# Kernel tuning notes

Measured on AMD Instinct MI355X. Metric: run time of the kernel, lower is better.

The kernel has to match this reference:

```python
import jax, jax.numpy as jnp
import numpy as np

# ---- static anchor construction (mirrors build_anchors + valid_index in __init__) ----
F_W, F_H, F_S = 50, 37, 16
SCALES = (8.0, 16.0, 24.0)
RATIOS = (0.5, 1.0, 2.0)
K1 = 400            # rp() top-k proposals fed to NMS
NMS_THRESH = 0.6
BN_EPS = 1e-5

def _build_anchors():
    anchors = []
    for y in range(F_H):
        for x in range(F_W):
            cx = x * F_S + F_S / 2.0
            cy = y * F_S + F_S / 2.0
            for r in RATIOS:           # 3 ratios x 3 scales = 9 anchors/cell (18 = 9*2 cls ch)
                for s in SCALES:
                    h = F_S * s * np.sqrt(r)
                    w = F_S * s / np.sqrt(r)
                    anchors.append([cx - w / 2, cy - h / 2, cx + w / 2, cy + h / 2])
    return np.asarray(anchors, dtype=np.float32)

_ANCH = _build_anchors()
_VALID = np.where((_ANCH[:, 0] >= 0) & (_ANCH[:, 1] >= 0) &
                  (_ANCH[:, 2] < F_W * F_S) & (_ANCH[:, 3] < F_H * F_S))[0]
VALID_ANCHOR = jnp.asarray(_ANCH[_VALID])   # [V, 4]
VALID_INDEX = jnp.asarray(_VALID)            # [V]


def _conv(x, w, b, pad):
    y = jax.lax.conv_general_dilated(x, w, (1, 1), [(pad, pad), (pad, pad)],
                                     dimension_numbers=('NCHW', 'OIHW', 'NCHW'))
    return y + b[None, :, None, None]


def _nms_keep(boxes, scores, thresh):
    """Greedy NMS over K1 boxes; returns bool keep mask aligned to input order."""
    n = boxes.shape[0]
    order = jnp.argsort(-scores)
    b = boxes[order]
    x1, y1, x2, y2 = b[:, 0], b[:, 1], b[:, 2], b[:, 3]
    area = (x2 - x1 + 1.0) * (y2 - y1 + 1.0)
    iw = jnp.clip(jnp.minimum(x2[:, None], x2[None, :]) - jnp.maximum(x1[:, None], x1[None, :]) + 1.0, 0.0)
    ih = jnp.clip(jnp.minimum(y2[:, None], y2[None, :]) - jnp.maximum(y1[:, None], y1[None, :]) + 1.0, 0.0)
    inter = iw * ih
    iou = inter / (area[:, None] + area[None, :] - inter)
    idx = jnp.arange(n)

    def body(i, supp):
        alive = ~supp[i]
        new = alive & (iou[i] > thresh) & (idx > i)
        return supp | new

    supp = jax.lax.fori_loop(0, n, body, jnp.zeros(n, dtype=bool))
    return jnp.zeros(n, dtype=bool).at[order].set(~supp)


def _rp_single(off_i, cls_i):
    """rp(): softmax fg score -> top-k1 -> box decode -> NMS keep mask."""
    off_v = off_i[VALID_INDEX]                       # [V, 4]
    cls_v = cls_i[VALID_INDEX]                       # [V, 2]
    score = jax.nn.softmax(cls_v, axis=1)[:, 1]
    top_s, top_idx = jax.lax.top_k(score, K1)
    a = VALID_ANCHOR[top_idx]
    t = off_v[top_idx]
    xa = (a[:, 0] + a[:, 2]) / 2
    ya = (a[:, 1] + a[:, 3]) / 2
    wa = a[:, 2] - a[:, 0] + 1.0
    ha = a[:, 3] - a[:, 1] + 1.0
    x = t[:, 0] * wa + xa
    y = t[:, 1] * ha + ya
    w = wa * jnp.exp(t[:, 2])
    h = ha * jnp.exp(t[:, 3])
    boxes = jnp.stack([x - w / 2, y - h / 2, x + w / 2, y + h / 2], axis=1)  # [K1, 4]
    keep = _nms_keep(jnp.trunc(boxes), top_s, NMS_THRESH)  # original casts to int before NMS
    return boxes, keep


def setup_inputs() -> dict:
    key = jax.random.key(0)
    ks = jax.random.split(key, 8)
    B = 8
    return {
        'feature': jax.random.normal(ks[0], (B, 512, F_H, F_W), jnp.float32),
        'md_w': jax.random.normal(ks[1], (512, 512, 3, 3), jnp.float32) * 0.02,
        'md_b': jax.random.normal(ks[2], (512,), jnp.float32) * 0.01,
        'bn_gamma': jnp.ones((512,), jnp.float32),
        'bn_beta': jnp.zeros((512,), jnp.float32),
        'cls_w': jax.random.normal(ks[3], (18, 512, 1, 1), jnp.float32) * 0.02,
        'cls_b': jax.random.normal(ks[4], (18,), jnp.float32) * 0.01,
        'off_w': jax.random.normal(ks[5], (36, 512, 1, 1), jnp.float32) * 0.02,
        'off_b': jax.random.normal(ks[6], (36,), jnp.float32) * 0.01,
    }


def reference(feature, md_w, md_b, bn_gamma, bn_beta, cls_w, cls_b, off_w, off_b):
    B = feature.shape[0]
    # more_deep: Conv3x3 -> BatchNorm (training-mode batch stats) -> ReLU
    out = _conv(feature, md_w, md_b, pad=1)
    mean = out.mean(axis=(0, 2, 3), keepdims=True)
    var = out.var(axis=(0, 2, 3), keepdims=True)
    out = bn_gamma[None, :, None, None] * (out - mean) * jax.lax.rsqrt(var + BN_EPS) + bn_beta[None, :, None, None]
    out = jax.nn.relu(out)
    # 1x1 heads, then permute(0,2,3,1).reshape as in predict()
    cls = _conv(out, cls_w, cls_b, pad=0)   # [B,18,H,W]
    off = _conv(out, off_w, off_b, pad=0)   # [B,36,H,W]
    cls_pred = cls.transpose(0, 2, 3, 1).reshape(B, -1, 2)   # [B, H*W*9, 2]
    offset_pred = off.transpose(0, 2, 3, 1).reshape(B, -1, 4)  # [B, H*W*9, 4]
    boxes, keep = jax.vmap(_rp_single)(offset_pred, cls_pred)  # [B,K1,4], [B,K1] bool
    return offset_pred, cls_pred, boxes, keep
```

## Files before the change

kernel.cpp:

```cpp
#include <hip/hip_runtime.h>
#include <cstdint>

#define BHW_ 14800
#define CHW_ 947200
#define A_   16650
#define OCLS 532800
#define OBOX 799200
#define OKEEP 812000
#define NSTEP 144

typedef unsigned int u32;
typedef unsigned long long u64;
typedef _Float16 f16x8 __attribute__((ext_vector_type(8)));
typedef float f32x4 __attribute__((ext_vector_type(4)));

__device__ __forceinline__ unsigned int fkey(float f){
  unsigned int u = __float_as_uint(f);
  return (u & 0x80000000u) ? ~u : (u | 0x80000000u);
}

__device__ __forceinline__ void anchor_corners(int x, int y, int kk,
                                               float& ax1, float& ay1, float& ax2, float& ay2){
  int si = kk % 3, ri = kk / 3;
  double rv = (ri==0) ? 0.5 : ((ri==1) ? 1.0 : 2.0);
  double sr = sqrt(rv);
  double fs = 128.0 * (double)(si+1);
  double h = fs * sr, w = fs / sr;
  double cx = (double)(x*16 + 8), cy = (double)(y*16 + 8);
  ax1 = (float)(cx - w*0.5); ay1 = (float)(cy - h*0.5);
  ax2 = (float)(cx + w*0.5); ay2 = (float)(cy + h*0.5);
}

__global__ __launch_bounds__(256) void k_split_w(const float* __restrict__ w,
                                                 const float* __restrict__ cw, const float* __restrict__ cb,
                                                 const float* __restrict__ ow, const float* __restrict__ ob,
                                                 _Float16* __restrict__ WfA,
                                                 float* __restrict__ hwp, float* __restrict__ hb){
  int bid = blockIdx.x;
  if (bid < 1152){
    int u = bid*256 + threadIdx.x;
    int khw = u % 9;
    int v = u / 9;
    int o7  = v & 127;
    int l4g = (v >> 7) & 3;
    int ot  = (v >> 9) & 3;
    int cc  = v >> 11;
    int o = ot*128 + o7;
    int s = cc*9 + khw;
    f16x8 hi, lo;
    #pragma unroll
    for (int j = 0; j < 8; ++j){
      float val = w[(size_t)(o*512 + cc*32 + l4g*8 + j)*9 + khw];
      _Float16 h = (_Float16)val;
      hi[j] = h; lo[j] = (_Float16)(val - (float)h);
    }
    size_t base = ((size_t)(s*4 + ot)*1024 + (size_t)(l4g*2)*128 + o7)*8;
    *(f16x8*)&WfA[base] = hi;
    *(f16x8*)&WfA[base + 1024] = lo;
  } else {
    int t = (bid - 1152)*256 + threadIdx.x;
    if (t < 64) hb[t] = (t < 18) ? cb[t] : (t < 54 ? ob[t-18] : 0.f);
    int r = t & 63, ci = t >> 6;
    hwp[t] = (r < 18) ? cw[r*512 + ci] : (r < 54 ? ow[(r-18)*512 + ci] : 0.f);
  }
}

__global__ __launch_bounds__(256) void k_split_f(const float* __restrict__ feat,
                                                 _Float16* __restrict__ Fph, _Float16* __restrict__ Fpl){
  int bid = blockIdx.x;
  if (bid < 928){
    __shared__ float T[64][129];
    int ct = bid & 3; int pt = (bid >> 2) % 29; int b = bid / 116;
    int tid = threadIdx.x;
    #pragma unroll
    for (int it = 0; it < 32; ++it){
      int idx = it*256 + tid;
      int c = idx >> 6, p = idx & 63;
      int pos = pt*64 + p;
      T[p][c] = (pos < 1850) ? feat[(size_t)(b*512 + ct*128 + c)*1850 + pos] : 0.f;
    }
    __syncthreads();
    #pragma unroll
    for (int it = 0; it < 4; ++it){
      int idx = it*256 + tid;
      int p = idx >> 4, c8 = (idx & 15) * 8;
      int pos = pt*64 + p;
      if (pos < 1850){
        int y = pos/50, x = pos - y*50;
        size_t off = ((size_t)(b*39 + y + 1)*52 + (x + 1))*512 + ct*128 + c8;
        f16x8 hv, lv;
        #pragma unroll
        for (int j = 0; j < 8; ++j){
          float v = T[p][c8 + j];
          _Float16 h = (_Float16)v;
          hv[j] = h; lv[j] = (_Float16)(v - (float)h);
        }
        *(f16x8*)&Fph[off] = hv;
        *(f16x8*)&Fpl[off] = lv;
      }
    }
  } else {
    int t = (bid - 928)*256 + threadIdx.x;
    if (t >= 182272) return;
    _Float16* base = (t < 91136) ? Fph : Fpl;
    int u = (t < 91136) ? t : t - 91136;
    int c8 = (u & 63) * 8;
    int pu = u >> 6;
    int b = pu / 178, p = pu - b*178;
    int yp, xp;
    if (p < 52){ yp = 0; xp = p; }
    else if (p < 104){ yp = 38; xp = p - 52; }
    else if (p < 141){ yp = p - 104 + 1; xp = 0; }
    else { yp = p - 141 + 1; xp = 51; }
    f16x8 z = {};
    *(f16x8*)&base[((size_t)(b*39 + yp)*52 + xp)*512 + c8] = z;
  }
}

__global__ __launch_bounds__(512, 2) void k_conv3_mfma(const _Float16* __restrict__ Fph,
                                                       const _Float16* __restrict__ Fpl,
                                                       const _Float16* __restrict__ WfA,
                                                       const float* __restrict__ mdb,
                                                       float* __restrict__ out0){
  __shared__ _Float16 Abuf[2][8192];
  __shared__ _Float16 Bbuf[2][8192];
  const int tid = threadIdx.x;
  int flat = blockIdx.x;
  int xcd = flat & 7, sub = flat >> 3;
  int swz = xcd * 58 + sub;
  int otile = swz / 116;
  int ntile = swz - otile*116;

  const int bpos = tid & 127, kg8 = tid >> 7;
  int n = ntile*128 + bpos; if (n >= BHW_) n = BHW_ - 1;
  int nb = n/1850; int rem = n - nb*1850; int ny = rem/50; int nx = rem - ny*50;
  const size_t pbase = ((size_t)(nb*39 + ny + 1)*52 + (nx + 1))*512 + kg8*8;

  auto stage = [&](int s, int cur){
    const _Float16* g = WfA + ((size_t)(s*4 + otile)*1024 + tid)*8;
    _Float16* la = &Abuf[cur][(size_t)tid*8];
    __builtin_amdgcn_global_load_lds((const __attribute__((address_space(1))) void*)g,
                                     (__attribute__((address_space(3))) void*)la, 16, 0, 0);
    __builtin_amdgcn_global_load_lds((const __attribute__((address_space(1))) void*)(g + 4096),
                                     (__attribute__((address_space(3))) void*)(la + 4096), 16, 0, 0);
    int cc = s/9, khw = s - cc*9;
    int dy = khw/3 - 1, dx = khw - (khw/3)*3 - 1;
    size_t src = pbase + (size_t)((dy*52 + dx)*512 + cc*32);
    _Float16* lb = &Bbuf[cur][(size_t)((kg8*2)*128 + bpos)*8];
    __builtin_amdgcn_global_load_lds((const __attribute__((address_space(1))) void*)(Fph + src),
                                     (__attribute__((address_space(3))) void*)lb, 16, 0, 0);
    __builtin_amdgcn_global_load_lds((const __attribute__((address_space(1))) void*)(Fpl + src),
                                     (__attribute__((address_space(3))) void*)(lb + 1024), 16, 0, 0);
  };

  const int w = tid >> 6, lane = tid & 63;
  const int wm = w >> 2, wn = w & 3;
  const int l15 = lane & 15, l4 = lane >> 4;

  f32x4 acc[4][2] = {};

  auto compute = [&](int cur){
    f16x8 ah[4], al[4], bh[2], bl[2];
    #pragma unroll
    for (int mf = 0; mf < 4; ++mf){
      int m = wm*64 + mf*16 + l15;
      ah[mf] = *(const f16x8*)&Abuf[cur][(size_t)((l4*2 + 0)*128 + m)*8];
      al[mf] = *(const f16x8*)&Abuf[cur][(size_t)((l4*2 + 1)*128 + m)*8];
    }
    #pragma unroll
    for (int nf = 0; nf < 2; ++nf){
      int nn = wn*32 + nf*16 + l15;
      bh[nf] = *(const f16x8*)&Bbuf[cur][(size_t)((l4*2 + 0)*128 + nn)*8];
      bl[nf] = *(const f16x8*)&Bbuf[cur][(size_t)((l4*2 + 1)*128 + nn)*8];
    }
    #pragma unroll
    for (int mf = 0; mf < 4; ++mf)
      #pragma unroll
      for (int nf = 0; nf < 2; ++nf){
        acc[mf][nf] = __builtin_amdgcn_mfma_f32_16x16x32_f16(ah[mf], bh[nf], acc[mf][nf], 0,0,0);
        acc[mf][nf] = __builtin_amdgcn_mfma_f32_16x16x32_f16(ah[mf], bl[nf], acc[mf][nf], 0,0,0);
        acc[mf][nf] = __builtin_amdgcn_mfma_f32_16x16x32_f16(al[mf], bh[nf], acc[mf][nf], 0,0,0);
      }
  };

  stage(0, 0);
  __syncthreads();
  int cur = 0;
  for (int s = 0; s < NSTEP; ++s){
    if (s + 1 < NSTEP){
      stage(s+1, cur^1);
      __builtin_amdgcn_sched_barrier(0);
    }
    compute(cur);
    __syncthreads();
    cur ^= 1;
  }

  #pragma unroll
  for (int nf = 0; nf < 2; ++nf){
    int ng = ntile*128 + wn*32 + nf*16 + l15;
    if (ng >= BHW_) continue;
    int b2 = ng/1850; int rem2 = ng - b2*1850;
    #pragma unroll
    for (int mf = 0; mf < 4; ++mf){
      int o0 = otile*128 + wm*64 + mf*16 + l4*4;
      #pragma unroll
      for (int r = 0; r < 4; ++r){
        out0[(size_t)b2*CHW_ + (size_t)(o0 + r)*1850 + rem2] = acc[mf][nf][r] + mdb[o0 + r];
      }
    }
  }
}

__global__ __launch_bounds__(256) void k_bnstats(const float* __restrict__ out0,
                                                 float* __restrict__ bnm, float* __restrict__ bnr){
  __shared__ double s1[256], s2[256];
  int c = blockIdx.x, tid = threadIdx.x;
  double a = 0.0, b = 0.0;
  for (int i = tid; i < BHW_; i += 256){
    int bb = i / 1850; int r = i - bb*1850;
    float v = out0[(size_t)bb*CHW_ + (size_t)c*1850 + r];
    a += (double)v; b += (double)v*(double)v;
  }
  s1[tid] = a; s2[tid] = b; __syncthreads();
  for (int off = 128; off; off >>= 1){
    if (tid < off){ s1[tid] += s1[tid+off]; s2[tid] += s2[tid+off]; }
    __syncthreads();
  }
  if (tid == 0){
    double m = s1[0] / 14800.0;
    double var = s2[0] / 14800.0 - m*m;
    bnm[c] = (float)m;
    bnr[c] = 1.0f / sqrtf((float)var + 1e-5f);
  }
}

__global__ __launch_bounds__(256) void k_heads(const float* __restrict__ out0, const float* __restrict__ hwp,
                                               const float* __restrict__ hb, const float* __restrict__ bnm,
                                               const float* __restrict__ bnr, const float* __restrict__ gamma,
                                               const float* __restrict__ beta, float* __restrict__ dout,
                                               u64* __restrict__ keys){
#pragma clang fp contract(off)
  __shared__ float As[16][64];
  __shared__ float Bs[16][64];
  __shared__ int sb[64], sy[64], sx[64];
  int tid = threadIdx.x; int ntile = blockIdx.x;
  if (tid < 64){
    int n = ntile*64 + tid;
    if (n < BHW_){ int b = n/1850; int r = n - b*1850; int y = r/50; sb[tid]=b; sy[tid]=y; sx[tid]=r - y*50; }
    else { sb[tid] = -1; sy[tid] = 0; sx[tid] = 0; }
  }
  __syncthreads();
  float acc[4][4] = {};
  const int tx = tid & 15, ty = tid >> 4;
  const int lci = tid >> 4, lo4 = (tid & 15) * 4;
  for (int ct = 0; ct < 32; ++ct){
    int cib = ct*16;
    float4 av = *(const float4*)(hwp + (cib + lci)*64 + lo4);
    float4 bv; float* bp = (float*)&bv;
    int cig = cib + lci;
    float gm = gamma[cig], mm = bnm[cig], rr = bnr[cig], bt = beta[cig];
    #pragma unroll
    for (int j = 0; j < 4; ++j){
      int nn = lo4 + j; int b = sb[nn];
      float v = 0.f;
      if (b >= 0){
        float x = out0[(size_t)b*CHW_ + (size_t)cig*1850 + sy[nn]*50 + sx[nn]];
        float y = gm * (x - mm);
        y = y * rr;
        y = y + bt;
        v = fmaxf(y, 0.f);
      }
      bp[j] = v;
    }
    __syncthreads();
    *(float4*)&As[lci][lo4] = av;
    *(float4*)&Bs[lci][lo4] = bv;
    __syncthreads();
    #pragma unroll
    for (int k = 0; k < 16; ++k){
      float4 a4 = *(const float4*)&As[k][ty*4];
      float4 b4 = *(const float4*)&Bs[k][tx*4];
      const float* ap = (const float*)&a4; const float* bq = (const float*)&b4;
      #pragma unroll
      for (int i = 0; i < 4; ++i)
        #pragma unroll
        for (int j = 0; j < 4; ++j)
          acc[i][j] = fmaf(ap[i], bq[j], acc[i][j]);
    }
  }
  #pragma unroll
  for (int i = 0; i < 4; ++i){
    int r = ty*4 + i;
    if (r >= 54) continue;
    float bias = hb[r];
    #pragma unroll
    for (int j = 0; j < 4; ++j){
      int nl = tx*4 + j;
      int b = sb[nl];
      if (b < 0) continue;
      int pos = sy[nl]*50 + sx[nl];
      float v = acc[i][j] + bias;
      if (r < 18){
        int kk = r >> 1, cc = r & 1;
        dout[OCLS + ((size_t)b*A_ + pos*9 + kk)*2 + cc] = v;
      } else {
        int r2 = r - 18, kk = r2 >> 2, cc = r2 & 3;
        dout[((size_t)b*A_ + pos*9 + kk)*4 + cc] = v;
      }
    }
  }
  if (ty < 5){
    #pragma unroll
    for (int i = 0; i < 4; i += 2){
      int r = ty*4 + i;
      if (r >= 18) continue;
      int kk = r >> 1;
      float b0 = hb[r], b1 = hb[r+1];
      #pragma unroll
      for (int j = 0; j < 4; ++j){
        int nl = tx*4 + j;
        int b = sb[nl];
        if (b < 0) continue;
        float c0 = acc[i][j] + b0;
        float c1 = acc[i+1][j] + b1;
        float d = c1 - c0;
        float ax1, ay1, ax2, ay2;
        anchor_corners(sx[nl], sy[nl], kk, ax1, ay1, ax2, ay2);
        bool valid = (ax1 >= 0.f) && (ay1 >= 0.f) && (ax2 < 800.f) && (ay2 < 592.f);
        unsigned a = (unsigned)(sy[nl]*50 + sx[nl])*9u + (unsigned)kk;
        u64 key = valid ? (((u64)fkey(d) << 32) | (u64)(~a)) : 0ull;
        keys[(size_t)b*A_ + a] = key;
      }
    }
  }
}

__global__ __launch_bounds__(1024) void k_post(const u64* __restrict__ keys,
                                               float* __restrict__ dout){
#pragma clang fp contract(off)
  __shared__ u32 hist[4096];
  __shared__ u32 sp[1024];
  __shared__ u64 selbuf[4096];
  __shared__ u64 stopk[400];
  __shared__ u32 adj32[6400];
  __shared__ float X1[400], Y1[400], X2[400], Y2[400], AR[400];
  __shared__ u32 ssup[13];
  __shared__ u32 s_t1, s_base1, s_t2, scnt;
  int b = blockIdx.x, tid = threadIdx.x;
  const u64* kb = keys + (size_t)b*A_;

  for (int i = tid; i < 4096; i += 1024) hist[i] = 0u;
  if (tid == 0) scnt = 0u;
  __syncthreads();
  for (int i = tid; i < A_; i += 1024){
    u64 k = kb[i];
    if (k) atomicAdd(&hist[(u32)(k >> 52)], 1u);
  }
  __syncthreads();
  {
    u32 p = hist[tid*4] + hist[tid*4+1] + hist[tid*4+2] + hist[tid*4+3];
    sp[tid] = p; __syncthreads();
    for (int off = 1; off < 1024; off <<= 1){
      u32 v = sp[tid] + ((tid + off < 1024) ? sp[tid + off] : 0u);
      __syncthreads(); sp[tid] = v; __syncthreads();
    }
    if (sp[tid] >= 400u && (tid == 1023 || sp[tid+1] < 400u)){
      u32 cum = (tid == 1023) ? 0u : sp[tid+1];
      for (int bb = tid*4 + 3; bb >= tid*4; --bb){
        cum += hist[bb];
        if (cum >= 400u){ s_t1 = (u32)bb; s_base1 = cum - hist[bb]; break; }
      }
    }
  }
  __syncthreads();
  const u32 t1 = s_t1;
  const u32 need2 = 400u - s_base1;

  __syncthreads();
  for (int i = tid; i < 4096; i += 1024) hist[i] = 0u;
  __syncthreads();
  for (int i = tid; i < A_; i += 1024){
    u64 k = kb[i];
    if (k && (u32)(k >> 52) == t1) atomicAdd(&hist[(u32)(k >> 40) & 0xFFFu], 1u);
  }
  __syncthreads();
  {
    u32 p = hist[tid*4] + hist[tid*4+1] + hist[tid*4+2] + hist[tid*4+3];
    sp[tid] = p; __syncthreads();
    for (int off = 1; off < 1024; off <<= 1){
      u32 v = sp[tid] + ((tid + off < 1024) ? sp[tid + off] : 0u);
      __syncthreads(); sp[tid] = v; __syncthreads();
    }
    if (sp[tid] >= need2 && (tid == 1023 || sp[tid+1] < need2)){
      u32 cum = (tid == 1023) ? 0u : sp[tid+1];
      for (int bb = tid*4 + 3; bb >= tid*4; --bb){
        cum += hist[bb];
        if (cum >= need2){ s_t2 = (u32)bb; break; }
      }
    }
  }
  __syncthreads();
  const u32 t2 = s_t2;

  for (int i = tid; i < A_; i += 1024){
    u64 k = kb[i];
    if (!k) continue;
    u32 top = (u32)(k >> 52);
    bool sel = (top > t1) || (top == t1 && ((u32)(k >> 40) & 0xFFFu) >= t2);
    if (sel){
      u32 pidx = atomicAdd(&scnt, 1u);
      if (pidx < 4096u) selbuf[pidx] = k;
    }
  }
  __syncthreads();
  int C = min((int)scnt, 4096);

  for (int i = tid; i < C; i += 1024){
    u64 my = selbuf[i];
    int c = 0;
    for (int j = 0; j < C; ++j) c += (selbuf[j] > my) ? 1 : 0;
    if (c < 400) stopk[c] = my;
  }
  __syncthreads();

  for (int i = tid; i < 6400; i += 1024) adj32[i] = 0u;
  if (tid < 400){
    u64 key = stopk[tid];
    unsigned a = ~(unsigned)(key & 0xFFFFFFFFull);
    int pos = a/9; int kk = a - pos*9;
    int y = pos/50; int x = pos - y*50;
    float ax1, ay1, ax2, ay2;
    anchor_corners(x, y, kk, ax1, ay1, ax2, ay2);
    float xa = (ax1 + ax2) * 0.5f;
    float ya = (ay1 + ay2) * 0.5f;
    float wa = ax2 - ax1 + 1.0f;
    float ha = ay2 - ay1 + 1.0f;
    const float* t = dout + ((size_t)b*A_ + a)*4;
    float t0 = t[0], t1f = t[1], t2f = t[2], t3 = t[3];
    float xc = t0 * wa + xa;
    float yc = t1f * ha + ya;
    float bw = wa * expf(t2f);
    float bh = ha * expf(t3);
    float bx1 = xc - bw*0.5f, by1 = yc - bh*0.5f;
    float bx2 = xc + bw*0.5f, by2 = yc + bh*0.5f;
    float* bo = dout + OBOX + ((size_t)b*400 + tid)*4;
    bo[0] = bx1; bo[1] = by1; bo[2] = bx2; bo[3] = by2;
    float tx1 = truncf(bx1), ty1 = truncf(by1), tx2 = truncf(bx2), ty2 = truncf(by2);
    X1[tid] = tx1; Y1[tid] = ty1; X2[tid] = tx2; Y2[tid] = ty2;
    AR[tid] = (tx2 - tx1 + 1.0f) * (ty2 - ty1 + 1.0f);
  }
  __syncthreads();
  for (int q = tid; q < 160000; q += 1024){
    int i = q / 400, j = q - i*400;
    if (j > i){
      float iw = fminf(X2[i], X2[j]) - fmaxf(X1[i], X1[j]) + 1.0f; iw = fmaxf(iw, 0.f);
      float ih = fminf(Y2[i], Y2[j]) - fmaxf(Y1[i], Y1[j]) + 1.0f; ih = fmaxf(ih, 0.f);
      float inter = iw * ih;
      float iou = inter / ((AR[i] + AR[j]) - inter);
      if (iou > 0.6f) atomicOr(&adj32[i*16 + (j >> 5)], 1u << (j & 31));
    }
  }
  __syncthreads();
  if (tid < 64){
    u32 sup = 0;
    for (int i = 0; i < 399; ++i){
      u32 a = (tid < 13) ? adj32[i*16 + tid] : 0u;
      u32 so = __shfl(sup, i >> 5);
      if (!((so >> (i & 31)) & 1u)) sup |= a;
    }
    if (tid < 13) ssup[tid] = sup;
  }
  __syncthreads();
  if (tid < 400)
    dout[OKEEP + (size_t)b*400 + tid] = ((ssup[tid >> 5] >> (tid & 31)) & 1u) ? 0.f : 1.f;
}

extern "C" void kernel_launch(void* const* d_in, const int* in_sizes, int n_in,
                              void* d_out, int out_size, void* d_ws, size_t ws_size,
                              hipStream_t stream){
  const float* feat  = (const float*)d_in[0];
  const float* mdw   = (const float*)d_in[1];
  const float* mdb   = (const float*)d_in[2];
  const float* gamma = (const float*)d_in[3];
  const float* beta  = (const float*)d_in[4];
  const float* clsw  = (const float*)d_in[5];
  const float* clsb  = (const float*)d_in[6];
  const float* offw  = (const float*)d_in[7];
  const float* offb  = (const float*)d_in[8];
  float* dout = (float*)d_out;
  float* ws = (float*)d_ws;

  float* out0 = ws;
  _Float16* WfA = (_Float16*)(out0 + 7577600);
  _Float16* Fph = (_Float16*)(out0 + 7577600 + 2359296);
  _Float16* Fpl = (_Float16*)(out0 + 7577600 + 2359296 + 4153344);
  float* hwp = out0 + 18243584;
  float* hb  = hwp + 32768;
  float* bnm = hb + 64;
  float* bnr = bnm + 512;
  u64* keys = (u64*)(bnr + 512);

  k_split_w<<<dim3(1280), 256, 0, stream>>>(mdw, clsw, clsb, offw, offb, WfA, hwp, hb);
  k_split_f<<<dim3(1640), 256, 0, stream>>>(feat, Fph, Fpl);
  k_conv3_mfma<<<dim3(464), 512, 0, stream>>>(Fph, Fpl, WfA, mdb, out0);
  k_bnstats<<<dim3(512), 256, 0, stream>>>(out0, bnm, bnr);
  k_heads<<<dim3(232), 256, 0, stream>>>(out0, hwp, hb, bnm, bnr, gamma, beta, dout, keys);
  k_post<<<dim3(8), 1024, 0, stream>>>(keys, dout);
}
```

Baseline: 408.3 us.

## Widen conv3 N tile to 256 and triple-buffer feature loads

```diff
diff --git a/kernel.cpp b/kernel.cpp
--- a/kernel.cpp
+++ b/kernel.cpp
@@ -117,88 +117,104 @@
   }
 }
 
-__global__ __launch_bounds__(512, 2) void k_conv3_mfma(const _Float16* __restrict__ Fph,
+__global__ __launch_bounds__(512, 1) void k_conv3_mfma(const _Float16* __restrict__ Fph,
                                                        const _Float16* __restrict__ Fpl,
                                                        const _Float16* __restrict__ WfA,
                                                        const float* __restrict__ mdb,
                                                        float* __restrict__ out0){
   __shared__ _Float16 Abuf[2][8192];
-  __shared__ _Float16 Bbuf[2][8192];
+  __shared__ _Float16 Bbuf[3][16384];
   const int tid = threadIdx.x;
   int flat = blockIdx.x;
   int xcd = flat & 7, sub = flat >> 3;
-  int swz = xcd * 58 + sub;
-  int otile = swz / 116;
-  int ntile = swz - otile*116;
-
-  const int bpos = tid & 127, kg8 = tid >> 7;
-  int n = ntile*128 + bpos; if (n >= BHW_) n = BHW_ - 1;
+  int swz = xcd * 29 + sub;
+  int otile = swz / 58;
+  int ntile = swz - otile*58;
+
+  const int p = tid & 255, kg = tid >> 8;
+  int n = ntile*256 + p; if (n >= BHW_) n = BHW_ - 1;
   int nb = n/1850; int rem = n - nb*1850; int ny = rem/50; int nx = rem - ny*50;
-  const size_t pbase = ((size_t)(nb*39 + ny + 1)*52 + (nx + 1))*512 + kg8*8;
-
-  auto stage = [&](int s, int cur){
+  const size_t pbase = ((size_t)(nb*39 + ny + 1)*52 + (nx + 1))*512 + kg*16;
+
+  auto stageA = [&](int s, int ab){
     const _Float16* g = WfA + ((size_t)(s*4 + otile)*1024 + tid)*8;
-    _Float16* la = &Abuf[cur][(size_t)tid*8];
+    _Float16* la = &Abuf[ab][(size_t)tid*8];
     __builtin_amdgcn_global_load_lds((const __attribute__((address_space(1))) void*)g,
                                      (__attribute__((address_space(3))) void*)la, 16, 0, 0);
     __builtin_amdgcn_global_load_lds((const __attribute__((address_space(1))) void*)(g + 4096),
                                      (__attribute__((address_space(3))) void*)(la + 4096), 16, 0, 0);
+  };
+  auto stageB = [&](int s, int bb){
     int cc = s/9, khw = s - cc*9;
     int dy = khw/3 - 1, dx = khw - (khw/3)*3 - 1;
     size_t src = pbase + (size_t)((dy*52 + dx)*512 + cc*32);
-    _Float16* lb = &Bbuf[cur][(size_t)((kg8*2)*128 + bpos)*8];
+    _Float16* lb = &Bbuf[bb][(size_t)((4*kg)*256 + p)*8];
     __builtin_amdgcn_global_load_lds((const __attribute__((address_space(1))) void*)(Fph + src),
                                      (__attribute__((address_space(3))) void*)lb, 16, 0, 0);
     __builtin_amdgcn_global_load_lds((const __attribute__((address_space(1))) void*)(Fpl + src),
-                                     (__attribute__((address_space(3))) void*)(lb + 1024), 16, 0, 0);
+                                     (__attribute__((address_space(3))) void*)(lb + 2048), 16, 0, 0);
+    __builtin_amdgcn_global_load_lds((const __attribute__((address_space(1))) void*)(Fph + src + 8),
+                                     (__attribute__((address_space(3))) void*)(lb + 4096), 16, 0, 0);
+    __builtin_amdgcn_global_load_lds((const __attribute__((address_space(1))) void*)(Fpl + src + 8),
+                                     (__attribute__((address_space(3))) void*)(lb + 6144), 16, 0, 0);
   };
 
   const int w = tid >> 6, lane = tid & 63;
   const int wm = w >> 2, wn = w & 3;
   const int l15 = lane & 15, l4 = lane >> 4;
 
-  f32x4 acc[4][2] = {};
-
-  auto compute = [&](int cur){
-    f16x8 ah[4], al[4], bh[2], bl[2];
+  f32x4 acc[4][4] = {};
+
+  auto compute = [&](int ab, int bb){
+    f16x8 ah[4], al[4], bh[4], bl[4];
     #pragma unroll
     for (int mf = 0; mf < 4; ++mf){
       int m = wm*64 + mf*16 + l15;
-      ah[mf] = *(const f16x8*)&Abuf[cur][(size_t)((l4*2 + 0)*128 + m)*8];
-      al[mf] = *(const f16x8*)&Abuf[cur][(size_t)((l4*2 + 1)*128 + m)*8];
-    }
-    #pragma unroll
-    for (int nf = 0; nf < 2; ++nf){
-      int nn = wn*32 + nf*16 + l15;
-      bh[nf] = *(const f16x8*)&Bbuf[cur][(size_t)((l4*2 + 0)*128 + nn)*8];
-      bl[nf] = *(const f16x8*)&Bbuf[cur][(size_t)((l4*2 + 1)*128 + nn)*8];
+      ah[mf] = *(const f16x8*)&Abuf[ab][(size_t)((l4*2 + 0)*128 + m)*8];
+      al[mf] = *(const f16x8*)&Abuf[ab][(size_t)((l4*2 + 1)*128 + m)*8];
+    }
+    #pragma unroll
+    for (int nf = 0; nf < 4; ++nf){
+      int nn = wn*64 + nf*16 + l15;
+      bh[nf] = *(const f16x8*)&Bbuf[bb][(size_t)((l4*2 + 0)*256 + nn)*8];
+      bl[nf] = *(const f16x8*)&Bbuf[bb][(size_t)((l4*2 + 1)*256 + nn)*8];
     }
     #pragma unroll
     for (int mf = 0; mf < 4; ++mf)
       #pragma unroll
-      for (int nf = 0; nf < 2; ++nf){
+      for (int nf = 0; nf < 4; ++nf){
         acc[mf][nf] = __builtin_amdgcn_mfma_f32_16x16x32_f16(ah[mf], bh[nf], acc[mf][nf], 0,0,0);
         acc[mf][nf] = __builtin_amdgcn_mfma_f32_16x16x32_f16(ah[mf], bl[nf], acc[mf][nf], 0,0,0);
         acc[mf][nf] = __builtin_amdgcn_mfma_f32_16x16x32_f16(al[mf], bh[nf], acc[mf][nf], 0,0,0);
       }
   };
 
-  stage(0, 0);
-  __syncthreads();
-  int cur = 0;
+  stageA(0, 0);
+  stageB(0, 0);
+  stageB(1, 1);
+  __builtin_amdgcn_sched_barrier(0);
+  asm volatile("s_waitcnt vmcnt(4)" ::: "memory");
+  __builtin_amdgcn_s_barrier();
+
+  int bb0 = 0, bb1 = 1, bb2 = 2;
   for (int s = 0; s < NSTEP; ++s){
-    if (s + 1 < NSTEP){
-      stage(s+1, cur^1);
-      __builtin_amdgcn_sched_barrier(0);
-    }
-    compute(cur);
-    __syncthreads();
-    cur ^= 1;
+    bool moreA = (s + 1 < NSTEP);
+    bool moreB = (s + 2 < NSTEP);
+    if (moreA) stageA(s+1, (s+1) & 1);
+    __builtin_amdgcn_sched_barrier(0);
+    if (moreB) stageB(s+2, bb2);
+    __builtin_amdgcn_sched_barrier(0);
+    compute(s & 1, bb0);
+    __builtin_amdgcn_sched_barrier(0);
+    if (moreB) asm volatile("s_waitcnt vmcnt(4)" ::: "memory");
+    else       asm volatile("s_waitcnt vmcnt(0)" ::: "memory");
+    __builtin_amdgcn_s_barrier();
+    int t = bb0; bb0 = bb1; bb1 = bb2; bb2 = t;
   }
 
   #pragma unroll
-  for (int nf = 0; nf < 2; ++nf){
-    int ng = ntile*128 + wn*32 + nf*16 + l15;
+  for (int nf = 0; nf < 4; ++nf){
+    int ng = ntile*256 + wn*64 + nf*16 + l15;
     if (ng >= BHW_) continue;
     int b2 = ng/1850; int rem2 = ng - b2*1850;
     #pragma unroll
@@ -503,7 +519,7 @@
 
   k_split_w<<<dim3(1280), 256, 0, stream>>>(mdw, clsw, clsb, offw, offb, WfA, hwp, hb);
   k_split_f<<<dim3(1640), 256, 0, stream>>>(feat, Fph, Fpl);
-  k_conv3_mfma<<<dim3(464), 512, 0, stream>>>(Fph, Fpl, WfA, mdb, out0);
+  k_conv3_mfma<<<dim3(232), 512, 0, stream>>>(Fph, Fpl, WfA, mdb, out0);
   k_bnstats<<<dim3(512), 256, 0, stream>>>(out0, bnm, bnr);
   k_heads<<<dim3(232), 256, 0, stream>>>(out0, hwp, hb, bnm, bnr, gamma, beta, dout, keys);
   k_post<<<dim3(8), 1024, 0, stream>>>(keys, dout);
```

After: 541.2 us. 1.33x slower.

## Keep padded features channel-major as packed hi/lo words and transpose in conv staging

Applied to the files above, without the earlier changes.

```diff
diff --git a/kernel.cpp b/kernel.cpp
--- a/kernel.cpp
+++ b/kernel.cpp
@@ -13,6 +13,9 @@
 typedef unsigned long long u64;
 typedef _Float16 f16x8 __attribute__((ext_vector_type(8)));
 typedef float f32x4 __attribute__((ext_vector_type(4)));
+
+union U8 { f16x8 v; u32 u[4]; };
+union H2U { _Float16 f; unsigned short u; };
 
 __device__ __forceinline__ unsigned int fkey(float f){
   unsigned int u = __float_as_uint(f);
@@ -31,14 +34,32 @@
   ax2 = (float)(cx + w*0.5); ay2 = (float)(cy + h*0.5);
 }
 
-__global__ __launch_bounds__(256) void k_split_w(const float* __restrict__ w,
-                                                 const float* __restrict__ cw, const float* __restrict__ cb,
-                                                 const float* __restrict__ ow, const float* __restrict__ ob,
-                                                 _Float16* __restrict__ WfA,
-                                                 float* __restrict__ hwp, float* __restrict__ hb){
+__global__ __launch_bounds__(256) void k_prep(const float* __restrict__ feat, const float* __restrict__ mdw,
+                                              const float* __restrict__ cw, const float* __restrict__ cb,
+                                              const float* __restrict__ ow, const float* __restrict__ ob,
+                                              u32* __restrict__ Fp, _Float16* __restrict__ WfA,
+                                              float* __restrict__ hwp, float* __restrict__ hb){
   int bid = blockIdx.x;
-  if (bid < 1152){
-    int u = bid*256 + threadIdx.x;
+  if (bid < 8112){
+    int q = bid*256 + threadIdx.x;
+    int p4 = (q % 507)*4;
+    int bc = q / 507;
+    u32 outw[4];
+    #pragma unroll
+    for (int e = 0; e < 4; ++e){
+      int padpos = p4 + e;
+      int yp = padpos/52, xp = padpos - yp*52;
+      float v = 0.f;
+      int y = yp - 1, x = xp - 1;
+      if ((unsigned)y < 37u && (unsigned)x < 50u) v = feat[(size_t)bc*1850 + y*50 + x];
+      _Float16 h = (_Float16)v;
+      _Float16 l = (_Float16)(v - (float)h);
+      H2U hu, lu; hu.f = h; lu.f = l;
+      outw[e] = ((u32)lu.u << 16) | (u32)hu.u;
+    }
+    *(uint4*)&Fp[(size_t)bc*2028 + p4] = *(uint4*)outw;
+  } else if (bid < 9264){
+    int u = (bid - 8112)*256 + threadIdx.x;
     int khw = u % 9;
     int v = u / 9;
     int o7  = v & 127;
@@ -50,7 +71,7 @@
     f16x8 hi, lo;
     #pragma unroll
     for (int j = 0; j < 8; ++j){
-      float val = w[(size_t)(o*512 + cc*32 + l4g*8 + j)*9 + khw];
+      float val = mdw[(size_t)(o*512 + cc*32 + l4g*8 + j)*9 + khw];
       _Float16 h = (_Float16)val;
       hi[j] = h; lo[j] = (_Float16)(val - (float)h);
     }
@@ -58,67 +79,14 @@
     *(f16x8*)&WfA[base] = hi;
     *(f16x8*)&WfA[base + 1024] = lo;
   } else {
-    int t = (bid - 1152)*256 + threadIdx.x;
+    int t = (bid - 9264)*256 + threadIdx.x;
     if (t < 64) hb[t] = (t < 18) ? cb[t] : (t < 54 ? ob[t-18] : 0.f);
     int r = t & 63, ci = t >> 6;
     hwp[t] = (r < 18) ? cw[r*512 + ci] : (r < 54 ? ow[(r-18)*512 + ci] : 0.f);
   }
 }
 
-__global__ __launch_bounds__(256) void k_split_f(const float* __restrict__ feat,
-                                                 _Float16* __restrict__ Fph, _Float16* __restrict__ Fpl){
-  int bid = blockIdx.x;
-  if (bid < 928){
-    __shared__ float T[64][129];
-    int ct = bid & 3; int pt = (bid >> 2) % 29; int b = bid / 116;
-    int tid = threadIdx.x;
-    #pragma unroll
-    for (int it = 0; it < 32; ++it){
-      int idx = it*256 + tid;
-      int c = idx >> 6, p = idx & 63;
-      int pos = pt*64 + p;
-      T[p][c] = (pos < 1850) ? feat[(size_t)(b*512 + ct*128 + c)*1850 + pos] : 0.f;
-    }
-    __syncthreads();
-    #pragma unroll
-    for (int it = 0; it < 4; ++it){
-      int idx = it*256 + tid;
-      int p = idx >> 4, c8 = (idx & 15) * 8;
-      int pos = pt*64 + p;
-      if (pos < 1850){
-        int y = pos/50, x = pos - y*50;
-        size_t off = ((size_t)(b*39 + y + 1)*52 + (x + 1))*512 + ct*128 + c8;
-        f16x8 hv, lv;
-        #pragma unroll
-        for (int j = 0; j < 8; ++j){
-          float v = T[p][c8 + j];
-          _Float16 h = (_Float16)v;
-          hv[j] = h; lv[j] = (_Float16)(v - (float)h);
-        }
-        *(f16x8*)&Fph[off] = hv;
-        *(f16x8*)&Fpl[off] = lv;
-      }
-    }
-  } else {
-    int t = (bid - 928)*256 + threadIdx.x;
-    if (t >= 182272) return;
-    _Float16* base = (t < 91136) ? Fph : Fpl;
-    int u = (t < 91136) ? t : t - 91136;
-    int c8 = (u & 63) * 8;
-    int pu = u >> 6;
-    int b = pu / 178, p = pu - b*178;
-    int yp, xp;
-    if (p < 52){ yp = 0; xp = p; }
-    else if (p < 104){ yp = 38; xp = p - 52; }
-    else if (p < 141){ yp = p - 104 + 1; xp = 0; }
-    else { yp = p - 141 + 1; xp = 51; }
-    f16x8 z = {};
-    *(f16x8*)&base[((size_t)(b*39 + yp)*52 + xp)*512 + c8] = z;
-  }
-}
-
-__global__ __launch_bounds__(512, 2) void k_conv3_mfma(const _Float16* __restrict__ Fph,
-                                                       const _Float16* __restrict__ Fpl,
+__global__ __launch_bounds__(512, 2) void k_conv3_mfma(const u32* __restrict__ Fp,
                                                        const _Float16* __restrict__ WfA,
                                                        const float* __restrict__ mdb,
                                                        float* __restrict__ out0){
@@ -134,23 +102,34 @@
   const int bpos = tid & 127, kg8 = tid >> 7;
   int n = ntile*128 + bpos; if (n >= BHW_) n = BHW_ - 1;
   int nb = n/1850; int rem = n - nb*1850; int ny = rem/50; int nx = rem - ny*50;
-  const size_t pbase = ((size_t)(nb*39 + ny + 1)*52 + (nx + 1))*512 + kg8*8;
-
-  auto stage = [&](int s, int cur){
-    const _Float16* g = WfA + ((size_t)(s*4 + otile)*1024 + tid)*8;
-    _Float16* la = &Abuf[cur][(size_t)tid*8];
-    __builtin_amdgcn_global_load_lds((const __attribute__((address_space(1))) void*)g,
-                                     (__attribute__((address_space(3))) void*)la, 16, 0, 0);
-    __builtin_amdgcn_global_load_lds((const __attribute__((address_space(1))) void*)(g + 4096),
-                                     (__attribute__((address_space(3))) void*)(la + 4096), 16, 0, 0);
+  const u32* bbase = Fp + (size_t)(nb*512 + kg8*8)*2028 + (ny+1)*52 + (nx+1);
+
+  u32 R[8];
+  auto loadB = [&](int s){
     int cc = s/9, khw = s - cc*9;
     int dy = khw/3 - 1, dx = khw - (khw/3)*3 - 1;
-    size_t src = pbase + (size_t)((dy*52 + dx)*512 + cc*32);
-    _Float16* lb = &Bbuf[cur][(size_t)((kg8*2)*128 + bpos)*8];
-    __builtin_amdgcn_global_load_lds((const __attribute__((address_space(1))) void*)(Fph + src),
-                                     (__attribute__((address_space(3))) void*)lb, 16, 0, 0);
-    __builtin_amdgcn_global_load_lds((const __attribute__((address_space(1))) void*)(Fpl + src),
-                                     (__attribute__((address_space(3))) void*)(lb + 1024), 16, 0, 0);
+    const u32* src = bbase + (size_t)cc*32*2028 + dy*52 + dx;
+    #pragma unroll
+    for (int i = 0; i < 8; ++i) R[i] = src[(size_t)i*2028];
+  };
+  auto writeB = [&](int cur){
+    U8 hi, lo;
+    #pragma unroll
+    for (int p = 0; p < 4; ++p){
+      u32 P0 = R[2*p], P1 = R[2*p+1];
+      hi.u[p] = (P1 << 16) | (P0 & 0xFFFFu);
+      lo.u[p] = (P0 >> 16) | (P1 & 0xFFFF0000u);
+    }
+    *(f16x8*)&Bbuf[cur][(size_t)((kg8*2 + 0)*128 + bpos)*8] = hi.v;
+    *(f16x8*)&Bbuf[cur][(size_t)((kg8*2 + 1)*128 + bpos)*8] = lo.v;
+  };
+  auto stageA = [&](int s, int cur){
+    const _Float16* g = WfA + ((size_t)(s*4 + otile)*1024 + tid)*8;
+    _Float16* l = &Abuf[cur][(size_t)tid*8];
+    __builtin_amdgcn_global_load_lds((const __attribute__((address_space(1))) void*)g,
+                                     (__attribute__((address_space(3))) void*)l, 16, 0, 0);
+    __builtin_amdgcn_global_load_lds((const __attribute__((address_space(1))) void*)(g + 4096),
+                                     (__attribute__((address_space(3))) void*)(l + 4096), 16, 0, 0);
   };
 
   const int w = tid >> 6, lane = tid & 63;
@@ -183,15 +162,20 @@
       }
   };
 
-  stage(0, 0);
-  __syncthreads();
+  loadB(0);
+  stageA(0, 0);
+  writeB(0);
+  __syncthreads();
+
   int cur = 0;
   for (int s = 0; s < NSTEP; ++s){
     if (s + 1 < NSTEP){
-      stage(s+1, cur^1);
+      loadB(s+1);
+      stageA(s+1, cur^1);
       __builtin_amdgcn_sched_barrier(0);
     }
     compute(cur);
+    if (s + 1 < NSTEP) writeB(cur^1);
     __syncthreads();
     cur ^= 1;
   }
@@ -493,17 +477,15 @@
 
   float* out0 = ws;
   _Float16* WfA = (_Float16*)(out0 + 7577600);
-  _Float16* Fph = (_Float16*)(out0 + 7577600 + 2359296);
-  _Float16* Fpl = (_Float16*)(out0 + 7577600 + 2359296 + 4153344);
-  float* hwp = out0 + 18243584;
+  u32* Fp = (u32*)(out0 + 7577600 + 2359296);
+  float* hwp = (float*)(Fp + 8306688);
   float* hb  = hwp + 32768;
   float* bnm = hb + 64;
   float* bnr = bnm + 512;
   u64* keys = (u64*)(bnr + 512);
 
-  k_split_w<<<dim3(1280), 256, 0, stream>>>(mdw, clsw, clsb, offw, offb, WfA, hwp, hb);
-  k_split_f<<<dim3(1640), 256, 0, stream>>>(feat, Fph, Fpl);
-  k_conv3_mfma<<<dim3(464), 512, 0, stream>>>(Fph, Fpl, WfA, mdb, out0);
+  k_prep<<<dim3(9392), 256, 0, stream>>>(feat, mdw, clsw, clsb, offw, offb, Fp, WfA, hwp, hb);
+  k_conv3_mfma<<<dim3(464), 512, 0, stream>>>(Fp, WfA, mdb, out0);
   k_bnstats<<<dim3(512), 256, 0, stream>>>(out0, bnm, bnr);
   k_heads<<<dim3(232), 256, 0, stream>>>(out0, hwp, hb, bnm, bnr, gamma, beta, dout, keys);
   k_post<<<dim3(8), 1024, 0, stream>>>(keys, dout);
```

Measured after the change: 389.5 us (median of 2 runs). -4.6%, faster.

## Triple-buffer feature tiles to prefetch two steps ahead in conv3 MFMA loop

Applied to the files above, without the earlier changes.

```diff
diff --git a/kernel.cpp b/kernel.cpp
--- a/kernel.cpp
+++ b/kernel.cpp
@@ -123,7 +123,7 @@
                                                        const float* __restrict__ mdb,
                                                        float* __restrict__ out0){
   __shared__ _Float16 Abuf[2][8192];
-  __shared__ _Float16 Bbuf[2][8192];
+  __shared__ _Float16 Bbuf[3][8192];
   const int tid = threadIdx.x;
   int flat = blockIdx.x;
   int xcd = flat & 7, sub = flat >> 3;
@@ -136,17 +136,19 @@
   int nb = n/1850; int rem = n - nb*1850; int ny = rem/50; int nx = rem - ny*50;
   const size_t pbase = ((size_t)(nb*39 + ny + 1)*52 + (nx + 1))*512 + kg8*8;
 
-  auto stage = [&](int s, int cur){
+  auto stageA = [&](int s, int ab){
     const _Float16* g = WfA + ((size_t)(s*4 + otile)*1024 + tid)*8;
-    _Float16* la = &Abuf[cur][(size_t)tid*8];
+    _Float16* la = &Abuf[ab][(size_t)tid*8];
     __builtin_amdgcn_global_load_lds((const __attribute__((address_space(1))) void*)g,
                                      (__attribute__((address_space(3))) void*)la, 16, 0, 0);
     __builtin_amdgcn_global_load_lds((const __attribute__((address_space(1))) void*)(g + 4096),
                                      (__attribute__((address_space(3))) void*)(la + 4096), 16, 0, 0);
+  };
+  auto stageB = [&](int s, int bb){
     int cc = s/9, khw = s - cc*9;
     int dy = khw/3 - 1, dx = khw - (khw/3)*3 - 1;
     size_t src = pbase + (size_t)((dy*52 + dx)*512 + cc*32);
-    _Float16* lb = &Bbuf[cur][(size_t)((kg8*2)*128 + bpos)*8];
+    _Float16* lb = &Bbuf[bb][(size_t)((kg8*2)*128 + bpos)*8];
     __builtin_amdgcn_global_load_lds((const __attribute__((address_space(1))) void*)(Fph + src),
                                      (__attribute__((address_space(3))) void*)lb, 16, 0, 0);
     __builtin_amdgcn_global_load_lds((const __attribute__((address_space(1))) void*)(Fpl + src),
@@ -159,19 +161,19 @@
 
   f32x4 acc[4][2] = {};
 
-  auto compute = [&](int cur){
+  auto compute = [&](int ab, int bb){
     f16x8 ah[4], al[4], bh[2], bl[2];
     #pragma unroll
     for (int mf = 0; mf < 4; ++mf){
       int m = wm*64 + mf*16 + l15;
-      ah[mf] = *(const f16x8*)&Abuf[cur][(size_t)((l4*2 + 0)*128 + m)*8];
-      al[mf] = *(const f16x8*)&Abuf[cur][(size_t)((l4*2 + 1)*128 + m)*8];
+      ah[mf] = *(const f16x8*)&Abuf[ab][(size_t)((l4*2 + 0)*128 + m)*8];
+      al[mf] = *(const f16x8*)&Abuf[ab][(size_t)((l4*2 + 1)*128 + m)*8];
     }
     #pragma unroll
     for (int nf = 0; nf < 2; ++nf){
       int nn = wn*32 + nf*16 + l15;
-      bh[nf] = *(const f16x8*)&Bbuf[cur][(size_t)((l4*2 + 0)*128 + nn)*8];
-      bl[nf] = *(const f16x8*)&Bbuf[cur][(size_t)((l4*2 + 1)*128 + nn)*8];
+      bh[nf] = *(const f16x8*)&Bbuf[bb][(size_t)((l4*2 + 0)*128 + nn)*8];
+      bl[nf] = *(const f16x8*)&Bbuf[bb][(size_t)((l4*2 + 1)*128 + nn)*8];
     }
     #pragma unroll
     for (int mf = 0; mf < 4; ++mf)
@@ -183,17 +185,22 @@
       }
   };
 
-  stage(0, 0);
-  __syncthreads();
-  int cur = 0;
+  stageA(0, 0);
+  stageB(0, 0);
+  stageB(1, 1);
+  __builtin_amdgcn_sched_barrier(0);
+  asm volatile("s_waitcnt vmcnt(2)" ::: "memory");
+  __builtin_amdgcn_s_barrier();
+
   for (int s = 0; s < NSTEP; ++s){
-    if (s + 1 < NSTEP){
-      stage(s+1, cur^1);
-      __builtin_amdgcn_sched_barrier(0);
-    }
-    compute(cur);
-    __syncthreads();
-    cur ^= 1;
+    if (s + 1 < NSTEP) stageA(s+1, (s+1) & 1);
+    if (s + 2 < NSTEP) stageB(s+2, (s+2) % 3);
+    __builtin_amdgcn_sched_barrier(0);
+    compute(s & 1, s % 3);
+    __builtin_amdgcn_sched_barrier(0);
+    if (s + 2 < NSTEP) asm volatile("s_waitcnt vmcnt(2)" ::: "memory");
+    else               asm volatile("s_waitcnt vmcnt(0)" ::: "memory");
+    __builtin_amdgcn_s_barrier();
   }
 
   #pragma unroll
```

Result: no change. 405.3 us (-0.7%).
